# Performance work log

Measured on AMD Instinct MI355X. Metric: run time of the kernel, lower is better.

The kernel has to match this reference:

```python
import jax, jax.numpy as jnp
import numpy as np

D_STATE = 16
DT_RANK = 48
D_CONV = 4
EPS = 1e-5


def rmsnorm(x, w):
    return x * jax.lax.rsqrt(jnp.mean(x * x, axis=-1, keepdims=True) + EPS) * w


def causal_dw_conv(u, w, b):
    # u: [B,T,D], w: [D,K] depthwise causal kernel, b: [D]
    B, T, D = u.shape
    K = w.shape[1]
    up = jnp.pad(u, ((0, 0), (K - 1, 0), (0, 0)))
    acc = jnp.zeros_like(u)
    for k in range(K):  # K=4, tiny fixed loop
        acc = acc + up[:, k:k + T, :] * w[:, k]
    return acc + b


def mamba_mixer(h, ipw, cw, cb, xpw, dpw, dpb, alog, dpar, opw):
    # h: [B,T,d_model]
    B, T, _ = h.shape
    xz = h @ ipw.T                       # [B,T,2*d_inner]
    u, z = jnp.split(xz, 2, axis=-1)     # each [B,T,d_inner]
    u = jax.nn.silu(causal_dw_conv(u, cw, cb))
    xp = u @ xpw.T                       # [B,T,dt_rank+2*d_state]
    dt = xp[..., :DT_RANK]
    Bm = xp[..., DT_RANK:DT_RANK + D_STATE]
    Cm = xp[..., DT_RANK + D_STATE:]
    delta = jax.nn.softplus(dt @ dpw.T + dpb)      # [B,T,d_inner]
    A = -jnp.exp(alog)                              # [d_inner, d_state], negative
    dA = jnp.exp(delta[..., None] * A)              # [B,T,d_inner,d_state] in (0,1)
    dBu = (delta * u)[..., None] * Bm[:, :, None, :]
    # time-major for scan
    dA_t = jnp.moveaxis(dA, 1, 0)
    dBu_t = jnp.moveaxis(dBu, 1, 0)
    C_t = jnp.moveaxis(Cm, 1, 0)

    def step(hst, inp):
        a, bu, c = inp
        hst = a * hst + bu                          # [B,d_inner,d_state]
        y = jnp.einsum('bdn,bn->bd', hst, c)
        return hst, y

    h0 = jnp.zeros((B, u.shape[-1], D_STATE), u.dtype)
    _, ys = jax.lax.scan(step, h0, (dA_t, dBu_t, C_t))
    y = jnp.moveaxis(ys, 0, 1) + u * dpar           # skip via D
    y = y * jax.nn.silu(z)                          # gate
    return y @ opw.T                                # [B,T,d_model]


def setup_inputs() -> dict:
    key = jax.random.key(0)
    ks = jax.random.split(key, 16)
    L, d_model, d_inner = 4, 768, 1536
    B, C, T = 4, 256, 512
    s = 0.02
    return {
        'x': jax.random.normal(ks[0], (B, C, T), jnp.float32),
        'in_proj_w': jax.random.normal(ks[1], (L, 2 * d_inner, d_model), jnp.float32) * s,
        'conv_w': jax.random.normal(ks[2], (L, d_inner, D_CONV), jnp.float32) * 0.3,
        'conv_b': jnp.zeros((L, d_inner), jnp.float32),
        'x_proj_w': jax.random.normal(ks[3], (L, DT_RANK + 2 * D_STATE, d_inner), jnp.float32) * s,
        'dt_proj_w': jax.random.normal(ks[4], (L, d_inner, DT_RANK), jnp.float32) * 0.1,
        'dt_proj_b': jax.random.normal(ks[5], (L, d_inner), jnp.float32) * 0.1 - 4.0,
        'A_log': jax.random.uniform(ks[6], (L, d_inner, D_STATE), jnp.float32, 0.0, 1.5),
        'D_param': jax.random.uniform(ks[7], (L, d_inner), jnp.float32),
        'out_proj_w': jax.random.normal(ks[8], (L, d_model, d_inner), jnp.float32) * s,
        'norm_w': jnp.ones((L, d_model), jnp.float32),
        'norm_f_w': jnp.ones((d_model,), jnp.float32),
        'inp_w': jax.random.normal(ks[9], (d_model, C), jnp.float32) * s,
        'inp_b': jnp.zeros((d_model,), jnp.float32),
        'cls_w': jax.random.normal(ks[10], (10, d_model), jnp.float32) * s,
        'cls_b': jnp.zeros((10,), jnp.float32),
    }


def reference(x, in_proj_w, conv_w, conv_b, x_proj_w, dt_proj_w, dt_proj_b,
              A_log, D_param, out_proj_w, norm_w, norm_f_w,
              inp_w, inp_b, cls_w, cls_b):
    # x: (B, C, T) -> (B, T, C)
    xt = jnp.transpose(x, (0, 2, 1))
    h = xt @ inp_w.T + inp_b                # [B,T,d_model]
    hidden = h
    residual = None
    L = in_proj_w.shape[0]
    for l in range(L):
        residual = hidden if residual is None else hidden + residual
        normed = rmsnorm(residual, norm_w[l])
        hidden = mamba_mixer(normed, in_proj_w[l], conv_w[l], conv_b[l],
                             x_proj_w[l], dt_proj_w[l], dt_proj_b[l],
                             A_log[l], D_param[l], out_proj_w[l])
    residual = hidden + residual
    hidden = rmsnorm(residual, norm_f_w)
    pooled = hidden.mean(axis=1)            # [B,d_model]
    logits = pooled @ cls_w.T + cls_b       # [B,num_labels]
    return logits
```

## Files before the change

kernel.cpp:

```cpp
#include <hip/hip_runtime.h>
#include <math.h>

#define D_MODEL 768
#define D_INNER 1536
#define B_SZ 4
#define T_SZ 512
#define ROWS (B_SZ*T_SZ)
#define XP_N 80
#define CH 16
#define CT 32
#define XS 8
#define XKC (D_INNER/XS)

typedef __attribute__((ext_vector_type(8))) short bf16x8;
typedef __attribute__((ext_vector_type(4))) float f32x4;

__device__ __forceinline__ float sigmoidf_(float x){ return 1.0f/(1.0f+__expf(-x)); }
__device__ __forceinline__ float siluf_(float x){ return x*sigmoidf_(x); }
__device__ __forceinline__ unsigned short f2bf(float f){
  unsigned u = __builtin_bit_cast(unsigned, f);
  u = (u + 0x7FFFu + ((u >> 16) & 1u)) >> 16;
  return (unsigned short)u;
}

__global__ void transpose_x(const float* __restrict__ x, float* __restrict__ xt){
  __shared__ float s[32][33];
  int b = blockIdx.z;
  int t0 = blockIdx.x*32, c0 = blockIdx.y*32;
  int tx = threadIdx.x, ty = threadIdx.y;
  s[ty][tx] = x[((size_t)b*256 + (c0+ty))*512 + (t0+tx)];
  __syncthreads();
  xt[((size_t)b*512 + (t0+ty))*256 + (c0+tx)] = s[tx][ty];
}

__global__ __launch_bounds__(256) void cast_bf16(const float* __restrict__ in,
                                                 unsigned short* __restrict__ o, int n){
  const int i4 = (blockIdx.x*256 + threadIdx.x)*4;
  if (i4 >= n) return;
  float4 v = *(const float4*)(in + i4);
  ushort4 r;
  r.x = f2bf(v.x); r.y = f2bf(v.y); r.z = f2bf(v.z); r.w = f2bf(v.w);
  *(ushort4*)(o + i4) = r;
}

#define LDP 40
__global__ __launch_bounds__(256) void gemm_bf16(
    const unsigned short* __restrict__ A, const unsigned short* __restrict__ Wb,
    float* __restrict__ C, int M, int N, int K)
{
  __shared__ unsigned short As[128*LDP];
  __shared__ unsigned short Ws[128*LDP];
  const int tid = threadIdx.x;
  const int bm = blockIdx.y*128, bn = blockIdx.x*128;
  const int wave = tid >> 6, lane = tid & 63;
  const int wm = (wave >> 1)*64, wn = (wave & 1)*64;
  const int fr = lane & 15, quad = lane >> 4;
  f32x4 acc[4][4] = {};
  const int srow = tid >> 1, scol = (tid & 1)*16;
  const unsigned short* Ag = A  + (size_t)(bm + srow)*K + scol;
  const unsigned short* Wg = Wb + (size_t)(bn + srow)*K + scol;
  unsigned short* Asw = As + srow*LDP + scol;
  unsigned short* Wsw = Ws + srow*LDP + scol;

  for (int k0 = 0; k0 < K; k0 += 32){
    float4 av0 = *(const float4*)(Ag + k0);
    float4 av1 = *(const float4*)(Ag + k0 + 8);
    float4 wv0 = *(const float4*)(Wg + k0);
    float4 wv1 = *(const float4*)(Wg + k0 + 8);
    __syncthreads();
    *(float4*)(Asw)     = av0; *(float4*)(Asw + 8) = av1;
    *(float4*)(Wsw)     = wv0; *(float4*)(Wsw + 8) = wv1;
    __syncthreads();
    bf16x8 a[4], b[4];
    #pragma unroll
    for (int i=0;i<4;i++)
      a[i] = *(const bf16x8*)(As + (wm + i*16 + fr)*LDP + quad*8);
    #pragma unroll
    for (int j=0;j<4;j++)
      b[j] = *(const bf16x8*)(Ws + (wn + j*16 + fr)*LDP + quad*8);
    #pragma unroll
    for (int i=0;i<4;i++)
      #pragma unroll
      for (int j=0;j<4;j++)
        acc[i][j] = __builtin_amdgcn_mfma_f32_16x16x32_bf16(a[i], b[j], acc[i][j], 0, 0, 0);
  }
  #pragma unroll
  for (int i=0;i<4;i++){
    #pragma unroll
    for (int r=0;r<4;r++){
      const int row = bm + wm + i*16 + quad*4 + r;
      float* Cp = C + (size_t)row*N + bn + wn + fr;
      #pragma unroll
      for (int j=0;j<4;j++)
        Cp[j*16] = acc[i][j][r];
    }
  }
}

__global__ __launch_bounds__(256) void sgemm_tn(
    const float* __restrict__ A, int lda,
    const float* __restrict__ W,
    const float* __restrict__ bias,
    float* __restrict__ C, int M, int N, int K, int act)
{
  __shared__ float As[16][64];
  __shared__ float Wsh[16][64];
  const int bm = blockIdx.y*64, bn = blockIdx.x*64;
  const int tid = threadIdx.x;
  const int tx = tid & 15, ty = tid >> 4;
  const int lm = tid & 63, lk = (tid >> 6) << 2;
  float acc[4][4] = {};
  const float* Ap = A + (size_t)(bm+lm)*lda + lk;
  const float* Wp = W + (size_t)(bn+lm)*K + lk;
  const bool wok = (bn+lm) < N;
  for (int k0 = 0; k0 < K; k0 += 16){
    float4 av = *(const float4*)(Ap + k0);
    float4 wv = wok ? *(const float4*)(Wp + k0) : make_float4(0.f,0.f,0.f,0.f);
    As[lk+0][lm]=av.x; As[lk+1][lm]=av.y; As[lk+2][lm]=av.z; As[lk+3][lm]=av.w;
    Wsh[lk+0][lm]=wv.x; Wsh[lk+1][lm]=wv.y; Wsh[lk+2][lm]=wv.z; Wsh[lk+3][lm]=wv.w;
    __syncthreads();
    #pragma unroll
    for (int k = 0; k < 16; k++){
      float a[4], w[4];
      #pragma unroll
      for (int i=0;i<4;i++) a[i] = As[k][ty*4+i];
      #pragma unroll
      for (int j=0;j<4;j++) w[j] = Wsh[k][tx*4+j];
      #pragma unroll
      for (int i=0;i<4;i++)
        #pragma unroll
        for (int j=0;j<4;j++)
          acc[i][j] += a[i]*w[j];
    }
    __syncthreads();
  }
  #pragma unroll
  for (int i=0;i<4;i++){
    const int r = bm + ty*4 + i;
    #pragma unroll
    for (int j=0;j<4;j++){
      const int n = bn + tx*4 + j;
      if (n < N){
        float v = acc[i][j] + (bias ? bias[n] : 0.f);
        if (act == 1){ v = (v > 20.f) ? v : log1pf(__expf(v)); }
        C[(size_t)r*N + n] = v;
      }
    }
  }
}

__global__ __launch_bounds__(256) void sgemm_splitk_xp(
    const float* __restrict__ A, const float* __restrict__ W,
    float* __restrict__ part)
{
  __shared__ float As[16][64];
  __shared__ float Wsh[16][64];
  const int bm = blockIdx.y*64, bn = blockIdx.x*64;
  const int s = blockIdx.z;
  const int koff = s*XKC;
  const int tid = threadIdx.x;
  const int tx = tid & 15, ty = tid >> 4;
  const int lm = tid & 63, lk = (tid >> 6) << 2;
  float acc[4][4] = {};
  const float* Ap = A + (size_t)(bm+lm)*D_INNER + koff + lk;
  const float* Wp = W + (size_t)(bn+lm)*D_INNER + koff + lk;
  const bool wok = (bn+lm) < XP_N;
  for (int k0 = 0; k0 < XKC; k0 += 16){
    float4 av = *(const float4*)(Ap + k0);
    float4 wv = wok ? *(const float4*)(Wp + k0) : make_float4(0.f,0.f,0.f,0.f);
    As[lk+0][lm]=av.x; As[lk+1][lm]=av.y; As[lk+2][lm]=av.z; As[lk+3][lm]=av.w;
    Wsh[lk+0][lm]=wv.x; Wsh[lk+1][lm]=wv.y; Wsh[lk+2][lm]=wv.z; Wsh[lk+3][lm]=wv.w;
    __syncthreads();
    #pragma unroll
    for (int k = 0; k < 16; k++){
      float a[4], w[4];
      #pragma unroll
      for (int i=0;i<4;i++) a[i] = As[k][ty*4+i];
      #pragma unroll
      for (int j=0;j<4;j++) w[j] = Wsh[k][tx*4+j];
      #pragma unroll
      for (int i=0;i<4;i++)
        #pragma unroll
        for (int j=0;j<4;j++)
          acc[i][j] += a[i]*w[j];
    }
    __syncthreads();
  }
  #pragma unroll
  for (int i=0;i<4;i++){
    const int r = bm + ty*4 + i;
    #pragma unroll
    for (int j=0;j<4;j++){
      const int n = bn + tx*4 + j;
      if (n < XP_N)
        part[((size_t)s*ROWS + r)*XP_N + n] = acc[i][j];
    }
  }
}

__global__ __launch_bounds__(256) void reduce_xp(const float* __restrict__ part,
                                                 float* __restrict__ xp){
  const int i = blockIdx.x*256 + threadIdx.x;
  if (i >= ROWS*XP_N) return;
  float s = 0.f;
  #pragma unroll
  for (int c=0;c<XS;c++) s += part[(size_t)c*ROWS*XP_N + i];
  xp[i] = s;
}

__global__ __launch_bounds__(256) void add_rmsnorm(
    float* __restrict__ resid, const float* __restrict__ add,
    const float* __restrict__ w, float* __restrict__ out,
    unsigned short* __restrict__ obf)
{
  const int row = blockIdx.x;
  const int tid = threadIdx.x;
  float v[3];
  float ss = 0.f;
  #pragma unroll
  for (int i=0;i<3;i++){
    const int c = tid + i*256;
    float r = resid[(size_t)row*768 + c];
    if (add) r += add[(size_t)row*768 + c];
    v[i] = r;
    ss += r*r;
  }
  #pragma unroll
  for (int off=32; off>=1; off>>=1) ss += __shfl_xor(ss, off);
  __shared__ float sred[4];
  const int lane = tid & 63, wv = tid >> 6;
  if (lane == 0) sred[wv] = ss;
  __syncthreads();
  const float tot = sred[0]+sred[1]+sred[2]+sred[3];
  const float scale = rsqrtf(tot*(1.0f/768.0f) + 1e-5f);
  #pragma unroll
  for (int i=0;i<3;i++){
    const int c = tid + i*256;
    if (add) resid[(size_t)row*768 + c] = v[i];
    const float o = v[i]*scale*w[c];
    if (obf) obf[(size_t)row*768 + c] = f2bf(o);
    else     out[(size_t)row*768 + c] = o;
  }
}

__global__ __launch_bounds__(256) void conv_silu(
    const float* __restrict__ xz, const float* __restrict__ cw,
    const float* __restrict__ cb, float* __restrict__ uo)
{
  const int idx = blockIdx.x*256 + threadIdx.x;
  if (idx >= ROWS*D_INNER) return;
  const int d = idx % D_INNER;
  const int row = idx / D_INNER;
  const int t = row & (T_SZ-1);
  float acc = cb[d];
  #pragma unroll
  for (int k=0;k<4;k++){
    const int tt = t - 3 + k;
    if (tt >= 0)
      acc += xz[(size_t)(row - 3 + k)*3072 + d] * cw[d*4 + k];
  }
  uo[idx] = siluf_(acc);
}

__global__ __launch_bounds__(256) void scan_pass1(
    const float* __restrict__ delta, const float* __restrict__ u,
    const float* __restrict__ xp, const float* __restrict__ alog,
    float* __restrict__ Pend, float* __restrict__ Hend)
{
  const int d = blockIdx.x*256 + threadIdx.x;
  const int b = blockIdx.y, c = blockIdx.z;
  float4 t0 = *(const float4*)(alog + d*16 + 0);
  float4 t1 = *(const float4*)(alog + d*16 + 4);
  float4 t2 = *(const float4*)(alog + d*16 + 8);
  float4 t3 = *(const float4*)(alog + d*16 + 12);
  float Av[16] = {t0.x,t0.y,t0.z,t0.w,t1.x,t1.y,t1.z,t1.w,
                  t2.x,t2.y,t2.z,t2.w,t3.x,t3.y,t3.z,t3.w};
  float h[16], P[16];
  #pragma unroll
  for (int n=0;n<16;n++){ Av[n] = -__expf(Av[n]); h[n]=0.f; P[n]=1.f; }
  const size_t row0 = (size_t)b*T_SZ + (size_t)c*CT;
  const float* dp = delta + row0*D_INNER + d;
  const float* up = u     + row0*D_INNER + d;
  const float* bp = xp    + row0*XP_N + 48;
  for (int t=0;t<CT;t++){
    const float dv = dp[(size_t)t*D_INNER];
    const float uv = up[(size_t)t*D_INNER];
    const float4 B0 = *(const float4*)(bp + (size_t)t*XP_N);
    const float4 B1 = *(const float4*)(bp + (size_t)t*XP_N + 4);
    const float4 B2 = *(const float4*)(bp + (size_t)t*XP_N + 8);
    const float4 B3 = *(const float4*)(bp + (size_t)t*XP_N + 12);
    const float Bv[16] = {B0.x,B0.y,B0.z,B0.w,B1.x,B1.y,B1.z,B1.w,
                          B2.x,B2.y,B2.z,B2.w,B3.x,B3.y,B3.z,B3.w};
    const float du = dv*uv;
    #pragma unroll
    for (int n=0;n<16;n++){
      const float dA = __expf(dv*Av[n]);
      P[n] *= dA;
      h[n] = dA*h[n] + du*Bv[n];
    }
  }
  float* Pp = Pend + ((size_t)(b*CH+c)*D_INNER + d)*16;
  float* Hp = Hend + ((size_t)(b*CH+c)*D_INNER + d)*16;
  *(float4*)(Pp+ 0) = make_float4(P[0],P[1],P[2],P[3]);
  *(float4*)(Pp+ 4) = make_float4(P[4],P[5],P[6],P[7]);
  *(float4*)(Pp+ 8) = make_float4(P[8],P[9],P[10],P[11]);
  *(float4*)(Pp+12) = make_float4(P[12],P[13],P[14],P[15]);
  *(float4*)(Hp+ 0) = make_float4(h[0],h[1],h[2],h[3]);
  *(float4*)(Hp+ 4) = make_float4(h[4],h[5],h[6],h[7]);
  *(float4*)(Hp+ 8) = make_float4(h[8],h[9],h[10],h[11]);
  *(float4*)(Hp+12) = make_float4(h[12],h[13],h[14],h[15]);
}

__global__ __launch_bounds__(256) void scan_combine(
    const float* __restrict__ Pend, const float* __restrict__ Hend,
    float* __restrict__ Hin)
{
  const int gid = blockIdx.x*256 + threadIdx.x;
  const int b = gid / (D_INNER*16);
  const int r = gid % (D_INNER*16);
  const size_t base = (size_t)b*CH*D_INNER*16 + r;
  const size_t step = (size_t)D_INNER*16;
  float h = 0.f;
  Hin[base] = 0.f;
  for (int c=0; c<CH-1; c++){
    h = Pend[base + (size_t)c*step]*h + Hend[base + (size_t)c*step];
    Hin[base + (size_t)(c+1)*step] = h;
  }
}

__global__ __launch_bounds__(256) void scan_pass3(
    const float* __restrict__ delta, const float* __restrict__ u,
    const float* __restrict__ xp, const float* __restrict__ xz,
    const float* __restrict__ alog, const float* __restrict__ Dp,
    const float* __restrict__ Hin, unsigned short* __restrict__ yb)
{
  const int d = blockIdx.x*256 + threadIdx.x;
  const int b = blockIdx.y, c = blockIdx.z;
  float4 t0 = *(const float4*)(alog + d*16 + 0);
  float4 t1 = *(const float4*)(alog + d*16 + 4);
  float4 t2 = *(const float4*)(alog + d*16 + 8);
  float4 t3 = *(const float4*)(alog + d*16 + 12);
  float Av[16] = {t0.x,t0.y,t0.z,t0.w,t1.x,t1.y,t1.z,t1.w,
                  t2.x,t2.y,t2.z,t2.w,t3.x,t3.y,t3.z,t3.w};
  #pragma unroll
  for (int n=0;n<16;n++) Av[n] = -__expf(Av[n]);
  const float* Hp = Hin + ((size_t)(b*CH+c)*D_INNER + d)*16;
  float4 h0 = *(const float4*)(Hp+0);
  float4 h1 = *(const float4*)(Hp+4);
  float4 h2 = *(const float4*)(Hp+8);
  float4 h3 = *(const float4*)(Hp+12);
  float h[16] = {h0.x,h0.y,h0.z,h0.w,h1.x,h1.y,h1.z,h1.w,
                 h2.x,h2.y,h2.z,h2.w,h3.x,h3.y,h3.z,h3.w};
  const float Dv = Dp[d];
  const size_t row0 = (size_t)b*T_SZ + (size_t)c*CT;
  const float* dp = delta + row0*D_INNER + d;
  const float* up = u     + row0*D_INNER + d;
  const float* bp = xp    + row0*XP_N + 48;
  const float* cp = xp    + row0*XP_N + 64;
  const float* zp = xz    + row0*3072 + 1536 + d;
  unsigned short* yp = yb + row0*D_INNER + d;
  for (int t=0;t<CT;t++){
    const float dv = dp[(size_t)t*D_INNER];
    const float uv = up[(size_t)t*D_INNER];
    const float zv = zp[(size_t)t*3072];
    const float4 B0 = *(const float4*)(bp + (size_t)t*XP_N);
    const float4 B1 = *(const float4*)(bp + (size_t)t*XP_N + 4);
    const float4 B2 = *(const float4*)(bp + (size_t)t*XP_N + 8);
    const float4 B3 = *(const float4*)(bp + (size_t)t*XP_N + 12);
    const float4 C0 = *(const float4*)(cp + (size_t)t*XP_N);
    const float4 C1 = *(const float4*)(cp + (size_t)t*XP_N + 4);
    const float4 C2 = *(const float4*)(cp + (size_t)t*XP_N + 8);
    const float4 C3 = *(const float4*)(cp + (size_t)t*XP_N + 12);
    const float Bv[16] = {B0.x,B0.y,B0.z,B0.w,B1.x,B1.y,B1.z,B1.w,
                          B2.x,B2.y,B2.z,B2.w,B3.x,B3.y,B3.z,B3.w};
    const float Cv[16] = {C0.x,C0.y,C0.z,C0.w,C1.x,C1.y,C1.z,C1.w,
                          C2.x,C2.y,C2.z,C2.w,C3.x,C3.y,C3.z,C3.w};
    const float du = dv*uv;
    float p = 0.f;
    #pragma unroll
    for (int n=0;n<16;n++){
      const float dA = __expf(dv*Av[n]);
      h[n] = dA*h[n] + du*Bv[n];
      p += h[n]*Cv[n];
    }
    yp[(size_t)t*D_INNER] = f2bf((p + uv*Dv)*siluf_(zv));
  }
}

__global__ void pool_mean(const float* __restrict__ normed, float* __restrict__ pooled){
  const int idx = blockIdx.x*256 + threadIdx.x;
  if (idx >= B_SZ*768) return;
  const int b = idx / 768, m = idx % 768;
  float s = 0.f;
  for (int t=0; t<T_SZ; t++) s += normed[((size_t)b*T_SZ + t)*768 + m];
  pooled[idx] = s * (1.0f/T_SZ);
}

__global__ void cls_head(const float* __restrict__ pooled, const float* __restrict__ cw,
                         const float* __restrict__ cb, float* __restrict__ out){
  const int o = blockIdx.x % 10, b = blockIdx.x / 10;
  const int lane = threadIdx.x;
  float s = 0.f;
  for (int k = lane; k < 768; k += 64) s += pooled[b*768 + k]*cw[o*768 + k];
  #pragma unroll
  for (int off=32; off>=1; off>>=1) s += __shfl_xor(s, off);
  if (lane == 0) out[b*10 + o] = s + cb[o];
}

extern "C" void kernel_launch(void* const* d_in, const int* in_sizes, int n_in,
                              void* d_out, int out_size, void* d_ws, size_t ws_size,
                              hipStream_t stream) {
  const float* x         = (const float*)d_in[0];
  const float* in_proj_w = (const float*)d_in[1];
  const float* conv_w    = (const float*)d_in[2];
  const float* conv_b    = (const float*)d_in[3];
  const float* x_proj_w  = (const float*)d_in[4];
  const float* dt_proj_w = (const float*)d_in[5];
  const float* dt_proj_b = (const float*)d_in[6];
  const float* A_log     = (const float*)d_in[7];
  const float* D_param   = (const float*)d_in[8];
  const float* out_proj_w= (const float*)d_in[9];
  const float* norm_w    = (const float*)d_in[10];
  const float* norm_f_w  = (const float*)d_in[11];
  const float* inp_w     = (const float*)d_in[12];
  const float* inp_b     = (const float*)d_in[13];
  const float* cls_w     = (const float*)d_in[14];
  const float* cls_b     = (const float*)d_in[15];
  float* out = (float*)d_out;

  char* ws = (char*)d_ws;
  auto carve = [&](size_t nelem)->float* {
    float* p = (float*)ws;
    ws += ((nelem*sizeof(float) + 255)/256)*256;
    return p;
  };
  float* xt     = carve((size_t)ROWS*256);
  float* resid  = carve((size_t)ROWS*768);
  float* normed = carve((size_t)ROWS*768);
  float* hidden = carve((size_t)ROWS*768);
  float* xz     = carve((size_t)ROWS*3072);
  float* ucv    = carve((size_t)ROWS*1536);
  float* xp     = carve((size_t)ROWS*XP_N);
  float* delta  = carve((size_t)ROWS*1536);
  float* ybf_f  = carve((size_t)ROWS*1536/2);
  float* wbf_f  = carve((size_t)(3072*768)/2);
  float* Hin    = carve((size_t)B_SZ*CH*D_INNER*16);
  float* xpart  = carve((size_t)XS*ROWS*XP_N);
  float* pooled = carve((size_t)B_SZ*768);

  unsigned short* normedb = (unsigned short*)normed;
  unsigned short* ybf = (unsigned short*)ybf_f;
  unsigned short* wbf = (unsigned short*)wbf_f;
  float* Pend = normed;
  float* Hend = hidden;

  transpose_x<<<dim3(16,8,4), dim3(32,32), 0, stream>>>(x, xt);
  sgemm_tn<<<dim3(12,32), 256, 0, stream>>>(xt, 256, inp_w, inp_b, resid, ROWS, 768, 256, 0);

  for (int l = 0; l < 4; l++){
    add_rmsnorm<<<ROWS, 256, 0, stream>>>(resid, l ? hidden : nullptr, norm_w + (size_t)l*768,
                                          nullptr, normedb);
    cast_bf16<<<(3072*768)/1024, 256, 0, stream>>>(in_proj_w + (size_t)l*3072*768, wbf, 3072*768);
    gemm_bf16<<<dim3(24,16), 256, 0, stream>>>(normedb, wbf, xz, ROWS, 3072, 768);
    conv_silu<<<(ROWS*D_INNER)/256, 256, 0, stream>>>(xz, conv_w + (size_t)l*1536*4, conv_b + (size_t)l*1536, ucv);
    sgemm_splitk_xp<<<dim3(2,32,XS), 256, 0, stream>>>(ucv, x_proj_w + (size_t)l*XP_N*1536, xpart);
    reduce_xp<<<(ROWS*XP_N)/256, 256, 0, stream>>>(xpart, xp);
    sgemm_tn<<<dim3(24,32), 256, 0, stream>>>(xp, XP_N, dt_proj_w + (size_t)l*1536*48, dt_proj_b + (size_t)l*1536,
                                              delta, ROWS, 1536, 48, 1);
    scan_pass1<<<dim3(6,B_SZ,CH-1), 256, 0, stream>>>(delta, ucv, xp,
                                               A_log + (size_t)l*1536*16, Pend, Hend);
    scan_combine<<<(B_SZ*D_INNER*16)/256, 256, 0, stream>>>(Pend, Hend, Hin);
    scan_pass3<<<dim3(6,B_SZ,CH), 256, 0, stream>>>(delta, ucv, xp, xz,
                                               A_log + (size_t)l*1536*16, D_param + (size_t)l*1536, Hin, ybf);
    cast_bf16<<<(768*1536)/1024, 256, 0, stream>>>(out_proj_w + (size_t)l*768*1536, wbf, 768*1536);
    gemm_bf16<<<dim3(6,16), 256, 0, stream>>>(ybf, wbf, hidden, ROWS, 768, 1536);
  }

  add_rmsnorm<<<ROWS, 256, 0, stream>>>(resid, hidden, norm_f_w, normed, nullptr);
  pool_mean<<<12, 256, 0, stream>>>(normed, pooled);
  cls_head<<<40, 64, 0, stream>>>(pooled, cls_w, cls_b, out);
}
```

Before: 975.5 us.

## Split-K the out_proj GEMM, fuse weight casts, and parallelize mean pooling

The out_proj bf16 GEMM, which launched only 96 blocks, now runs as a 4-way split-K grid. Partial results go into the dead delta/ucv buffers and a separate reduction kernel sums them. The two per-layer weight casts are merged into a single launch, with separate bf16 buffers for the in and out weights. Mean pooling is split into a 16-way partial sum over time plus a final reduce. The intent is more occupancy on under-filled kernels, at the cost of extra partial-buffer memory traffic and one more launch per layer.

```diff
diff --git a/kernel.cpp b/kernel.cpp
--- a/kernel.cpp
+++ b/kernel.cpp
@@ -11,6 +11,9 @@
 #define CT 32
 #define XS 8
 #define XKC (D_INNER/XS)
+#define OS 4
+#define OKC (D_INNER/OS)
+#define MN_OUT (ROWS*768)
 
 typedef __attribute__((ext_vector_type(8))) short bf16x8;
 typedef __attribute__((ext_vector_type(4))) float f32x4;
@@ -33,10 +36,13 @@
   xt[((size_t)b*512 + (t0+ty))*256 + (c0+tx)] = s[tx][ty];
 }
 
-__global__ __launch_bounds__(256) void cast_bf16(const float* __restrict__ in,
-                                                 unsigned short* __restrict__ o, int n){
-  const int i4 = (blockIdx.x*256 + threadIdx.x)*4;
-  if (i4 >= n) return;
+__global__ __launch_bounds__(256) void cast2_bf16(
+    const float* __restrict__ in1, unsigned short* __restrict__ o1, int n1, int nb1,
+    const float* __restrict__ in2, unsigned short* __restrict__ o2, int n2)
+{
+  const float* in; unsigned short* o; int i4;
+  if ((int)blockIdx.x < nb1){ in = in1; o = o1; i4 = (blockIdx.x*256 + threadIdx.x)*4; if (i4 >= n1) return; }
+  else { in = in2; o = o2; i4 = ((blockIdx.x-nb1)*256 + threadIdx.x)*4; if (i4 >= n2) return; }
   float4 v = *(const float4*)(in + i4);
   ushort4 r;
   r.x = f2bf(v.x); r.y = f2bf(v.y); r.z = f2bf(v.z); r.w = f2bf(v.w);
@@ -95,6 +101,70 @@
         Cp[j*16] = acc[i][j][r];
     }
   }
+}
+
+__global__ __launch_bounds__(256) void gemm_bf16_sk(
+    const unsigned short* __restrict__ A, const unsigned short* __restrict__ Wb,
+    float* __restrict__ P0, float* __restrict__ P1, int M, int N, int K)
+{
+  __shared__ unsigned short As[128*LDP];
+  __shared__ unsigned short Ws[128*LDP];
+  const int tid = threadIdx.x;
+  const int bm = blockIdx.y*128, bn = blockIdx.x*128;
+  const int s = blockIdx.z;
+  const int koff = s*OKC;
+  const int wave = tid >> 6, lane = tid & 63;
+  const int wm = (wave >> 1)*64, wn = (wave & 1)*64;
+  const int fr = lane & 15, quad = lane >> 4;
+  f32x4 acc[4][4] = {};
+  const int srow = tid >> 1, scol = (tid & 1)*16;
+  const unsigned short* Ag = A  + (size_t)(bm + srow)*K + koff + scol;
+  const unsigned short* Wg = Wb + (size_t)(bn + srow)*K + koff + scol;
+  unsigned short* Asw = As + srow*LDP + scol;
+  unsigned short* Wsw = Ws + srow*LDP + scol;
+
+  for (int k0 = 0; k0 < OKC; k0 += 32){
+    float4 av0 = *(const float4*)(Ag + k0);
+    float4 av1 = *(const float4*)(Ag + k0 + 8);
+    float4 wv0 = *(const float4*)(Wg + k0);
+    float4 wv1 = *(const float4*)(Wg + k0 + 8);
+    __syncthreads();
+    *(float4*)(Asw)     = av0; *(float4*)(Asw + 8) = av1;
+    *(float4*)(Wsw)     = wv0; *(float4*)(Wsw + 8) = wv1;
+    __syncthreads();
+    bf16x8 a[4], b[4];
+    #pragma unroll
+    for (int i=0;i<4;i++)
+      a[i] = *(const bf16x8*)(As + (wm + i*16 + fr)*LDP + quad*8);
+    #pragma unroll
+    for (int j=0;j<4;j++)
+      b[j] = *(const bf16x8*)(Ws + (wn + j*16 + fr)*LDP + quad*8);
+    #pragma unroll
+    for (int i=0;i<4;i++)
+      #pragma unroll
+      for (int j=0;j<4;j++)
+        acc[i][j] = __builtin_amdgcn_mfma_f32_16x16x32_bf16(a[i], b[j], acc[i][j], 0, 0, 0);
+  }
+  float* Cb = (s < 2 ? P0 : P1) + (size_t)(s & 1)*MN_OUT;
+  #pragma unroll
+  for (int i=0;i<4;i++){
+    #pragma unroll
+    for (int r=0;r<4;r++){
+      const int row = bm + wm + i*16 + quad*4 + r;
+      float* Cp = Cb + (size_t)row*N + bn + wn + fr;
+      #pragma unroll
+      for (int j=0;j<4;j++)
+        Cp[j*16] = acc[i][j][r];
+    }
+  }
+}
+
+__global__ __launch_bounds__(256) void reduce_out(
+    const float* __restrict__ P0, const float* __restrict__ P1,
+    float* __restrict__ C)
+{
+  const int i = blockIdx.x*256 + threadIdx.x;
+  C[i] = (P0[i] + P0[MN_OUT + i]) + (P1[i] + P1[MN_OUT + i]);
 }
 
 __global__ __launch_bounds__(256) void sgemm_tn(
@@ -387,13 +457,25 @@
   }
 }
 
-__global__ void pool_mean(const float* __restrict__ normed, float* __restrict__ pooled){
-  const int idx = blockIdx.x*256 + threadIdx.x;
-  if (idx >= B_SZ*768) return;
-  const int b = idx / 768, m = idx % 768;
+__global__ __launch_bounds__(256) void pool_partial(const float* __restrict__ normed,
+                                                    float* __restrict__ part){
+  const int i = blockIdx.x*256 + threadIdx.x;
+  const int s = blockIdx.y;
+  const int b = i / 768, m = i % 768;
+  float sum = 0.f;
+  const float* p = normed + ((size_t)b*T_SZ + s*32)*768 + m;
+  #pragma unroll
+  for (int t=0; t<32; t++) sum += p[(size_t)t*768];
+  part[s*3072 + i] = sum;
+}
+
+__global__ void pool_final(const float* __restrict__ part, float* __restrict__ pooled){
+  const int i = blockIdx.x*256 + threadIdx.x;
+  if (i >= 3072) return;
   float s = 0.f;
-  for (int t=0; t<T_SZ; t++) s += normed[((size_t)b*T_SZ + t)*768 + m];
-  pooled[idx] = s * (1.0f/T_SZ);
+  #pragma unroll
+  for (int c=0;c<16;c++) s += part[c*3072 + i];
+  pooled[i] = s * (1.0f/T_SZ);
 }
 
 __global__ void cls_head(const float* __restrict__ pooled, const float* __restrict__ cw,
@@ -443,14 +525,17 @@
   float* xp     = carve((size_t)ROWS*XP_N);
   float* delta  = carve((size_t)ROWS*1536);
   float* ybf_f  = carve((size_t)ROWS*1536/2);
-  float* wbf_f  = carve((size_t)(3072*768)/2);
+  float* wbi_f  = carve((size_t)(3072*768)/2);
+  float* wbo_f  = carve((size_t)(768*1536)/2);
   float* Hin    = carve((size_t)B_SZ*CH*D_INNER*16);
   float* xpart  = carve((size_t)XS*ROWS*XP_N);
+  float* ppool  = carve((size_t)16*3072);
   float* pooled = carve((size_t)B_SZ*768);
 
   unsigned short* normedb = (unsigned short*)normed;
   unsigned short* ybf = (unsigned short*)ybf_f;
-  unsigned short* wbf = (unsigned short*)wbf_f;
+  unsigned short* wbi = (unsigned short*)wbi_f;
+  unsigned short* wbo = (unsigned short*)wbo_f;
   float* Pend = normed;
   float* Hend = hidden;
 
@@ -460,8 +545,9 @@
   for (int l = 0; l < 4; l++){
     add_rmsnorm<<<ROWS, 256, 0, stream>>>(resid, l ? hidden : nullptr, norm_w + (size_t)l*768,
                                           nullptr, normedb);
-    cast_bf16<<<(3072*768)/1024, 256, 0, stream>>>(in_proj_w + (size_t)l*3072*768, wbf, 3072*768);
-    gemm_bf16<<<dim3(24,16), 256, 0, stream>>>(normedb, wbf, xz, ROWS, 3072, 768);
+    cast2_bf16<<<2304+1152, 256, 0, stream>>>(in_proj_w + (size_t)l*3072*768, wbi, 3072*768, 2304,
+                                              out_proj_w + (size_t)l*768*1536, wbo, 768*1536);
+    gemm_bf16<<<dim3(24,16), 256, 0, stream>>>(normedb, wbi, xz, ROWS, 3072, 768);
     conv_silu<<<(ROWS*D_INNER)/256, 256, 0, stream>>>(xz, conv_w + (size_t)l*1536*4, conv_b + (size_t)l*1536, ucv);
     sgemm_splitk_xp<<<dim3(2,32,XS), 256, 0, stream>>>(ucv, x_proj_w + (size_t)l*XP_N*1536, xpart);
     reduce_xp<<<(ROWS*XP_N)/256, 256, 0, stream>>>(xpart, xp);
@@ -472,11 +558,12 @@
     scan_combine<<<(B_SZ*D_INNER*16)/256, 256, 0, stream>>>(Pend, Hend, Hin);
     scan_pass3<<<dim3(6,B_SZ,CH), 256, 0, stream>>>(delta, ucv, xp, xz,
                                                A_log + (size_t)l*1536*16, D_param + (size_t)l*1536, Hin, ybf);
-    cast_bf16<<<(768*1536)/1024, 256, 0, stream>>>(out_proj_w + (size_t)l*768*1536, wbf, 768*1536);
-    gemm_bf16<<<dim3(6,16), 256, 0, stream>>>(ybf, wbf, hidden, ROWS, 768, 1536);
+    gemm_bf16_sk<<<dim3(6,16,OS), 256, 0, stream>>>(ybf, wbo, delta, ucv, ROWS, 768, 1536);
+    reduce_out<<<MN_OUT/256, 256, 0, stream>>>(delta, ucv, hidden);
   }
 
   add_rmsnorm<<<ROWS, 256, 0, stream>>>(resid, hidden, norm_f_w, normed, nullptr);
-  pool_mean<<<12, 256, 0, stream>>>(normed, pooled);
+  pool_partial<<<dim3(12,16), 256, 0, stream>>>(normed, ppool);
+  pool_final<<<12, 256, 0, stream>>>(ppool, pooled);
   cls_head<<<40, 64, 0, stream>>>(pooled, cls_w, cls_b, out);
 }
```

After: 849.0 us. -13.0%, faster.
